# Performance work log

Measured on AMD Instinct MI355X. Metric: run time of the kernel, lower is better.

The kernel has to match this reference:

```python
import jax, jax.numpy as jnp
import numpy as np

B, S, H, D = 1, 4096, 16, 64   # batch, seq_len, heads, dim_head (hidden = H*D = 1024)
Q_CHUNK = 512                  # query chunk size; divides S


def setup_inputs() -> dict:
    key = jax.random.key(0)
    kq, kk, kv = jax.random.split(key, 3)
    shape = (B, S, H * D)
    return {
        "query": jax.random.normal(kq, shape, jnp.float32),
        "key": jax.random.normal(kk, shape, jnp.float32),
        "value": jax.random.normal(kv, shape, jnp.float32),
    }


def _heads_to_batch(x):
    # (b, s, h*d) -> (b*h, s, d), matching reshape_heads_to_batch_dim
    b, s, _ = x.shape
    return x.reshape(b, s, H, D).transpose(0, 2, 1, 3).reshape(b * H, s, D)


def _batch_to_heads(x, b):
    # (b*h, s, d) -> (b, s, h*d), matching reshape_batch_dim_to_heads
    bh, s, d = x.shape
    return x.reshape(b, H, s, d).transpose(0, 2, 1, 3).reshape(b, s, H * d)


def reference(query, key, value):
    """Memory-efficient attention path of AttentionOp.apply_attention_dot.

    Math: out = softmax(q k^T / sqrt(dim_head)) v per (batch*head).
    (The mem-efficient path scales by 1/sqrt(k_features); self.scale is unused there.)
    Computed in query chunks to avoid materializing the full [BH, S, S] scores,
    honoring the chunked structure of the original.
    """
    b = query.shape[0]
    q = _heads_to_batch(query) * (1.0 / jnp.sqrt(jnp.float32(D)))  # (BH, S, D)
    k = _heads_to_batch(key)
    v = _heads_to_batch(value)

    n_chunks = q.shape[1] // Q_CHUNK
    # (n_chunks, BH, Q_CHUNK, D)
    qc = q.reshape(-1, n_chunks, Q_CHUNK, D).transpose(1, 0, 2, 3)

    def attend_chunk(qi):
        scores = jnp.einsum("bqd,bkd->bqk", qi, k)        # (BH, C, S)
        probs = jax.nn.softmax(scores, axis=-1)           # stable online-softmax equiv.
        return jnp.einsum("bqk,bkd->bqd", probs, v)       # (BH, C, D)

    oc = jax.lax.map(attend_chunk, qc)                    # (n_chunks, BH, C, D)
    out = oc.transpose(1, 0, 2, 3).reshape(-1, n_chunks * Q_CHUNK, D)
    return _batch_to_heads(out, b)
```

## Files before the change

### kernel.cpp

```cpp
#include <hip/hip_runtime.h>
#include <stdint.h>

typedef __bf16 bf16;
typedef __bf16 bf16x8 __attribute__((ext_vector_type(8)));
typedef float  f32x16 __attribute__((ext_vector_type(16)));

#define S_LEN 4096
#define NHEAD 16
#define HID   1024
#define NTILE 64
#define TILEB 8192
#define QSCALE (0.125f * 1.44269504088896340736f)
#define EXP2F(x) __builtin_amdgcn_exp2f(x)

#define AS1 __attribute__((address_space(1)))
#define AS3 __attribute__((address_space(3)))

__device__ __forceinline__ void gload16(const void* g, void* l) {
    __builtin_amdgcn_global_load_lds((const AS1 uint32_t*)g, (AS3 uint32_t*)l, 16, 0, 0);
}

__device__ __forceinline__ uint32_t pack_bf16(float a, float b) {
    union { bf16 h[2]; uint32_t u; } x;
    x.h[0] = (bf16)a; x.h[1] = (bf16)b;
    return x.u;
}

__global__ __launch_bounds__(256)
void prepack_kernel(const float* __restrict__ Kg, const float* __restrict__ Vg,
                    char* __restrict__ Kb, char* __restrict__ Vb)
{
    const int tile = blockIdx.x, h = blockIdx.y;
    const int t = threadIdx.x;
    __shared__ float Vs[64][65];

    const int key = t >> 2, dq = (t & 3) * 16;
    const float* kp = Kg + (size_t)(tile * 64 + key) * HID + h * 64 + dq;
    const float* vp = Vg + (size_t)(tile * 64 + key) * HID + h * 64 + dq;
    float kv[16], vv[16];
    #pragma unroll
    for (int i = 0; i < 4; ++i) {
        *(float4*)(kv + 4 * i) = *(const float4*)(kp + 4 * i);
        *(float4*)(vv + 4 * i) = *(const float4*)(vp + 4 * i);
    }
    {
        char* kout = Kb + (size_t)(h * NTILE + tile) * TILEB;
        const int i = (t & 3) * 2 + (key >> 5);
        bf16x8 b0, b1;
        #pragma unroll
        for (int e = 0; e < 8; ++e) { b0[e] = (bf16)kv[e]; b1[e] = (bf16)kv[8 + e]; }
        *(bf16x8*)(kout + i * 1024 + (key & 31) * 16)        = b0;
        *(bf16x8*)(kout + i * 1024 + (32 + (key & 31)) * 16) = b1;
    }
    #pragma unroll
    for (int e = 0; e < 16; ++e) Vs[key][dq + e] = vv[e];
    __syncthreads();
    {
        const int d = t >> 2, kq = (t & 3) * 16;
        float tv[16];
        #pragma unroll
        for (int e = 0; e < 16; ++e) tv[e] = Vs[kq + e][d];
        char* vout = Vb + (size_t)(h * NTILE + tile) * TILEB;
        const int j = (t & 3) * 2 + (d >> 5);
        bf16x8 b0, b1;
        #pragma unroll
        for (int e = 0; e < 8; ++e) { b0[e] = (bf16)tv[e]; b1[e] = (bf16)tv[8 + e]; }
        *(bf16x8*)(vout + j * 1024 + (d & 31) * 16)        = b0;
        *(bf16x8*)(vout + j * 1024 + (32 + (d & 31)) * 16) = b1;
    }
}

__global__ __launch_bounds__(512, 2)
void fattn_kernel(const float* __restrict__ Qg,
                  const char* __restrict__ Kb,
                  const char* __restrict__ Vb,
                  float* __restrict__ Og)
{
    const int sb = (blockIdx.x & 7) * 32 + (blockIdx.x >> 3);
    const int h  = sb >> 4;
    const int qc = sb & 15;
    const int t  = threadIdx.x;
    const int w  = t >> 6;
    const int l  = t & 63;
    const int lq = l & 31;
    const int hi = l >> 5;

    __shared__ __attribute__((aligned(128))) char lds[4 * 16384];

    bf16x8 qf[4];
    {
        const float* qp = Qg + (size_t)(qc * 256 + w * 32 + lq) * HID + h * 64 + hi * 8;
        #pragma unroll
        for (int kc = 0; kc < 4; ++kc) {
            float tmp[8];
            *(float4*)(tmp)     = *(const float4*)(qp + kc * 16);
            *(float4*)(tmp + 4) = *(const float4*)(qp + kc * 16 + 4);
            #pragma unroll
            for (int e = 0; e < 8; ++e) qf[kc][e] = (bf16)(tmp[e] * QSCALE);
        }
    }

    f32x16 ot0, ot1;
    #pragma unroll
    for (int i = 0; i < 16; ++i) { ot0[i] = 0.f; ot1[i] = 0.f; }
    float lrun = 0.f;

    const int sw = w & 3;
    const char* const srcb = ((w < 4) ? Kb : Vb)
                           + (size_t)h * (NTILE * TILEB) + sw * 2048 + l * 16;
    const int dstoff = (w < 4 ? 0 : 8192) + sw * 2048;
    auto stage = [&](int tile) {
        const char* src = srcb + (size_t)tile * TILEB;
        char* dst = lds + (tile & 3) * 16384 + dstoff;
        gload16(src, dst);
        gload16(src + 1024, dst + 1024);
    };

    stage(0);
    stage(1);

    for (int it = 0; it < NTILE; ++it) {
        if (it < NTILE - 2) {
            stage(it + 2);
            asm volatile("s_waitcnt vmcnt(4)" ::: "memory");
        } else if (it == NTILE - 2) {
            asm volatile("s_waitcnt vmcnt(2)" ::: "memory");
        } else {
            asm volatile("s_waitcnt vmcnt(0)" ::: "memory");
        }
        __builtin_amdgcn_s_barrier();
        asm volatile("" ::: "memory");

        const char* kt = lds + (it & 3) * 16384;
        const char* vt = kt + 8192;

        #pragma unroll
        for (int khalf = 0; khalf < 2; ++khalf) {
            bf16x8 kfh[4];
            #pragma unroll
            for (int kc = 0; kc < 4; ++kc)
                kfh[kc] = *(const bf16x8*)(kt + (kc * 2 + khalf) * 1024 + l * 16);

            f32x16 sc;
            #pragma unroll
            for (int i = 0; i < 16; ++i) sc[i] = 0.f;
            __builtin_amdgcn_s_setprio(1);
            #pragma unroll
            for (int kc = 0; kc < 4; ++kc)
                sc = __builtin_amdgcn_mfma_f32_32x32x16_bf16(kfh[kc], qf[kc], sc, 0, 0, 0);
            __builtin_amdgcn_s_setprio(0);

            bf16x8 vfh[4];
            #pragma unroll
            for (int j = 0; j < 4; ++j)
                vfh[j] = *(const bf16x8*)(vt + (khalf * 4 + j) * 1024 + l * 16);

            {
                float pa = 0.f, pb = 0.f, pc = 0.f, pd = 0.f;
                #pragma unroll
                for (int i = 0; i < 16; i += 4) {
                    float p0 = EXP2F(sc[i]),     p1 = EXP2F(sc[i + 1]);
                    float p2 = EXP2F(sc[i + 2]), p3 = EXP2F(sc[i + 3]);
                    sc[i] = p0; sc[i + 1] = p1; sc[i + 2] = p2; sc[i + 3] = p3;
                    pa += p0; pb += p1; pc += p2; pd += p3;
                }
                lrun += (pa + pb) + (pc + pd);
            }

            auto pvchunk = [&](int eb, const bf16x8& v0, const bf16x8& v1) {
                uint32_t p0 = pack_bf16(sc[eb + 0], sc[eb + 1]);
                uint32_t p1 = pack_bf16(sc[eb + 2], sc[eb + 3]);
                uint32_t p2 = pack_bf16(sc[eb + 4], sc[eb + 5]);
                uint32_t p3 = pack_bf16(sc[eb + 6], sc[eb + 7]);
                asm volatile("v_permlane32_swap_b32 %0, %1" : "+v"(p0), "+v"(p2));
                asm volatile("v_permlane32_swap_b32 %0, %1" : "+v"(p1), "+v"(p3));
                union { uint32_t w4[4]; bf16x8 v; } pb;
                pb.w4[0] = p0; pb.w4[1] = p1; pb.w4[2] = p2; pb.w4[3] = p3;
                __builtin_amdgcn_s_setprio(1);
                ot0 = __builtin_amdgcn_mfma_f32_32x32x16_bf16(v0, pb.v, ot0, 0, 0, 0);
                ot1 = __builtin_amdgcn_mfma_f32_32x32x16_bf16(v1, pb.v, ot1, 0, 0, 0);
                __builtin_amdgcn_s_setprio(0);
            };
            pvchunk(0, vfh[0], vfh[1]);
            pvchunk(8, vfh[2], vfh[3]);
        }

        __builtin_amdgcn_s_barrier();
        asm volatile("" ::: "memory");
    }

    lrun += __shfl_xor(lrun, 32);

    __syncthreads();

    {
        char* const ob = lds + w * 8192;
        const float inv = 1.f / lrun;
        const int x = (lq & 7) << 4;
        #pragma unroll
        for (int r = 0; r < 16; ++r) {
            const int d0 = (r & 3) + 8 * (r >> 2) + 4 * hi;
            *(float*)(ob + ((lq * 256 + d0 * 4) ^ x))        = ot0[r] * inv;
            *(float*)(ob + ((lq * 256 + (32 + d0) * 4) ^ x)) = ot1[r] * inv;
        }
        const int row = l >> 1, half = l & 1;
        const int xr = (row & 7) << 4;
        float* op = Og + (size_t)(qc * 256 + w * 32 + row) * HID + h * 64 + half * 32;
        #pragma unroll
        for (int i = 0; i < 8; ++i) {
            float4 v = *(const float4*)(ob + ((row * 256 + half * 128 + i * 16) ^ xr));
            *(float4*)(op + i * 4) = v;
        }
    }
}

extern "C" void kernel_launch(void* const* d_in, const int* in_sizes, int n_in,
                              void* d_out, int out_size, void* d_ws, size_t ws_size,
                              hipStream_t stream) {
    const float* Q = (const float*)d_in[0];
    const float* K = (const float*)d_in[1];
    const float* V = (const float*)d_in[2];
    float* O = (float*)d_out;
    char* Kb = (char*)d_ws;
    char* Vb = (char*)d_ws + (size_t)NHEAD * NTILE * TILEB;
    dim3 pgrid(NTILE, NHEAD);
    prepack_kernel<<<pgrid, 256, 0, stream>>>(K, V, Kb, Vb);
    fattn_kernel<<<256, 512, 0, stream>>>(Q, Kb, Vb, O);
}
```

Measured before the change: 99.50 us.

## Software-pipeline PV MFMA of second key half across loop iterations

Restructures the attention inner loop so the P·V MFMAs for the second half of each key tile run in the next iteration, interleaved with the next tile's QK^T MFMAs. The exp, sum and bf16 pack of the scores move into their own stage, with a peeled prologue for tile 0 and a trailing P·V after the loop. The aim is to overlap the exp/pack VALU work and LDS reads with matrix-core work, so there are fewer MFMA dependency stalls. In exchange, more accumulators and fragments stay live, which raises register pressure under the 512-thread, 2-block launch bound and risks spills.

```diff
diff --git a/kernel.cpp b/kernel.cpp
--- a/kernel.cpp
+++ b/kernel.cpp
@@ -116,10 +116,86 @@
         gload16(src + 1024, dst + 1024);
     };
 
+    auto kload = [&](bf16x8* d, const char* kt, int khalf) {
+        #pragma unroll
+        for (int kc = 0; kc < 4; ++kc)
+            d[kc] = *(const bf16x8*)(kt + (kc * 2 + khalf) * 1024 + l * 16);
+    };
+    auto vload = [&](bf16x8* d, const char* vt, int khalf) {
+        #pragma unroll
+        for (int j = 0; j < 4; ++j)
+            d[j] = *(const bf16x8*)(vt + (khalf * 4 + j) * 1024 + l * 16);
+    };
+    auto qkt = [&](f32x16& sc, const bf16x8* kf) {
+        #pragma unroll
+        for (int i = 0; i < 16; ++i) sc[i] = 0.f;
+        __builtin_amdgcn_s_setprio(1);
+        #pragma unroll
+        for (int kc = 0; kc < 4; ++kc)
+            sc = __builtin_amdgcn_mfma_f32_32x32x16_bf16(kf[kc], qf[kc], sc, 0, 0, 0);
+        __builtin_amdgcn_s_setprio(0);
+    };
+    auto expsumpack = [&](f32x16& sc, uint32_t* pp) {
+        float pa = 0.f, pb = 0.f, pc = 0.f, pd = 0.f;
+        #pragma unroll
+        for (int i = 0; i < 16; i += 4) {
+            float p0 = EXP2F(sc[i]),     p1 = EXP2F(sc[i + 1]);
+            float p2 = EXP2F(sc[i + 2]), p3 = EXP2F(sc[i + 3]);
+            sc[i] = p0; sc[i + 1] = p1; sc[i + 2] = p2; sc[i + 3] = p3;
+            pa += p0; pb += p1; pc += p2; pd += p3;
+        }
+        lrun += (pa + pb) + (pc + pd);
+        #pragma unroll
+        for (int half = 0; half < 2; ++half) {
+            uint32_t p0 = pack_bf16(sc[half * 8 + 0], sc[half * 8 + 1]);
+            uint32_t p1 = pack_bf16(sc[half * 8 + 2], sc[half * 8 + 3]);
+            uint32_t p2 = pack_bf16(sc[half * 8 + 4], sc[half * 8 + 5]);
+            uint32_t p3 = pack_bf16(sc[half * 8 + 6], sc[half * 8 + 7]);
+            asm volatile("v_permlane32_swap_b32 %0, %1" : "+v"(p0), "+v"(p2));
+            asm volatile("v_permlane32_swap_b32 %0, %1" : "+v"(p1), "+v"(p3));
+            pp[half * 4 + 0] = p0; pp[half * 4 + 1] = p1;
+            pp[half * 4 + 2] = p2; pp[half * 4 + 3] = p3;
+        }
+    };
+    auto pv = [&](const uint32_t* pp, const bf16x8* vv) {
+        union { uint32_t w4[4]; bf16x8 v; } u0, u1;
+        u0.w4[0] = pp[0]; u0.w4[1] = pp[1]; u0.w4[2] = pp[2]; u0.w4[3] = pp[3];
+        u1.w4[0] = pp[4]; u1.w4[1] = pp[5]; u1.w4[2] = pp[6]; u1.w4[3] = pp[7];
+        __builtin_amdgcn_s_setprio(1);
+        ot0 = __builtin_amdgcn_mfma_f32_32x32x16_bf16(vv[0], u0.v, ot0, 0, 0, 0);
+        ot1 = __builtin_amdgcn_mfma_f32_32x32x16_bf16(vv[1], u0.v, ot1, 0, 0, 0);
+        ot0 = __builtin_amdgcn_mfma_f32_32x32x16_bf16(vv[2], u1.v, ot0, 0, 0, 0);
+        ot1 = __builtin_amdgcn_mfma_f32_32x32x16_bf16(vv[3], u1.v, ot1, 0, 0, 0);
+        __builtin_amdgcn_s_setprio(0);
+    };
+
+    uint32_t pC[8];
+    bf16x8   vC[4];
+    bf16x8   kf[4];
+    f32x16   scA, scB;
+    uint32_t pA[8];
+    bf16x8   vA[4];
+
     stage(0);
     stage(1);
 
-    for (int it = 0; it < NTILE; ++it) {
+    stage(2);
+    asm volatile("s_waitcnt vmcnt(4)" ::: "memory");
+    __builtin_amdgcn_s_barrier();
+    asm volatile("" ::: "memory");
+    {
+        const char* kt = lds;
+        const char* vt = kt + 8192;
+        kload(kf, kt, 0); qkt(scA, kf);
+        expsumpack(scA, pA); vload(vA, vt, 0);
+        kload(kf, kt, 1); qkt(scB, kf);
+        pv(pA, vA);
+        expsumpack(scB, pC); vload(vC, vt, 1);
+    }
+    __builtin_amdgcn_s_barrier();
+    asm volatile("" ::: "memory");
+
+    for (int it = 1; it < NTILE; ++it) {
         if (it < NTILE - 2) {
             stage(it + 2);
             asm volatile("s_waitcnt vmcnt(4)" ::: "memory");
@@ -134,60 +210,17 @@
         const char* kt = lds + (it & 3) * 16384;
         const char* vt = kt + 8192;
 
-        #pragma unroll
-        for (int khalf = 0; khalf < 2; ++khalf) {
-            bf16x8 kfh[4];
-            #pragma unroll
-            for (int kc = 0; kc < 4; ++kc)
-                kfh[kc] = *(const bf16x8*)(kt + (kc * 2 + khalf) * 1024 + l * 16);
-
-            f32x16 sc;
-            #pragma unroll
-            for (int i = 0; i < 16; ++i) sc[i] = 0.f;
-            __builtin_amdgcn_s_setprio(1);
-            #pragma unroll
-            for (int kc = 0; kc < 4; ++kc)
-                sc = __builtin_amdgcn_mfma_f32_32x32x16_bf16(kfh[kc], qf[kc], sc, 0, 0, 0);
-            __builtin_amdgcn_s_setprio(0);
-
-            bf16x8 vfh[4];
-            #pragma unroll
-            for (int j = 0; j < 4; ++j)
-                vfh[j] = *(const bf16x8*)(vt + (khalf * 4 + j) * 1024 + l * 16);
-
-            {
-                float pa = 0.f, pb = 0.f, pc = 0.f, pd = 0.f;
-                #pragma unroll
-                for (int i = 0; i < 16; i += 4) {
-                    float p0 = EXP2F(sc[i]),     p1 = EXP2F(sc[i + 1]);
-                    float p2 = EXP2F(sc[i + 2]), p3 = EXP2F(sc[i + 3]);
-                    sc[i] = p0; sc[i + 1] = p1; sc[i + 2] = p2; sc[i + 3] = p3;
-                    pa += p0; pb += p1; pc += p2; pd += p3;
-                }
-                lrun += (pa + pb) + (pc + pd);
-            }
-
-            auto pvchunk = [&](int eb, const bf16x8& v0, const bf16x8& v1) {
-                uint32_t p0 = pack_bf16(sc[eb + 0], sc[eb + 1]);
-                uint32_t p1 = pack_bf16(sc[eb + 2], sc[eb + 3]);
-                uint32_t p2 = pack_bf16(sc[eb + 4], sc[eb + 5]);
-                uint32_t p3 = pack_bf16(sc[eb + 6], sc[eb + 7]);
-                asm volatile("v_permlane32_swap_b32 %0, %1" : "+v"(p0), "+v"(p2));
-                asm volatile("v_permlane32_swap_b32 %0, %1" : "+v"(p1), "+v"(p3));
-                union { uint32_t w4[4]; bf16x8 v; } pb;
-                pb.w4[0] = p0; pb.w4[1] = p1; pb.w4[2] = p2; pb.w4[3] = p3;
-                __builtin_amdgcn_s_setprio(1);
-                ot0 = __builtin_amdgcn_mfma_f32_32x32x16_bf16(v0, pb.v, ot0, 0, 0, 0);
-                ot1 = __builtin_amdgcn_mfma_f32_32x32x16_bf16(v1, pb.v, ot1, 0, 0, 0);
-                __builtin_amdgcn_s_setprio(0);
-            };
-            pvchunk(0, vfh[0], vfh[1]);
-            pvchunk(8, vfh[2], vfh[3]);
-        }
+        kload(kf, kt, 0); qkt(scA, kf);
+        pv(pC, vC);
+        expsumpack(scA, pA); vload(vA, vt, 0);
+        kload(kf, kt, 1); qkt(scB, kf);
+        pv(pA, vA);
+        expsumpack(scB, pC); vload(vC, vt, 1);
 
         __builtin_amdgcn_s_barrier();
         asm volatile("" ::: "memory");
     }
+    pv(pC, vC);
 
     lrun += __shfl_xor(lrun, 32);
 
```

Measured after the change: 98.80 us. Within noise of the previous version (-0.7%).
